# Optimization experiments

Measured on AMD Instinct MI355X. Metric: run time of the kernel, lower is better.

## Reference

```python
import jax, jax.numpy as jnp
import numpy as np

ALPHA = 0.2  # LeakyReLU negative slope
NEG_INF = -9e15  # mask value used by the torch dense GAT layer

def _gat_layer(x, adj, W, a1, a2):
    # x: [N, F], W: [F, Fh], a1/a2: [Fh]
    Wh = x @ W                                   # [N, Fh]
    f1 = Wh @ a1                                 # [N] source scores
    f2 = Wh @ a2                                 # [N] dest scores
    e = jax.nn.leaky_relu(f1[:, None] + f2[None, :], ALPHA)  # [N, N]
    att = jnp.where(adj > 0, e, NEG_INF)
    att = jax.nn.softmax(att, axis=1)
    return att @ Wh                              # [N, Fh]

def setup_inputs():
    key = jax.random.key(0)
    ks = jax.random.split(key, 8)
    N, F, H, Fh, C = 6144, 512, 4, 64, 40
    x = jax.random.normal(ks[0], (N, F), jnp.float32)
    # sparse-ish binary adjacency with self loops (dense storage as in the module)
    adj = (jax.random.uniform(ks[1], (N, N)) < 0.005).astype(jnp.float32)
    adj = jnp.maximum(adj, jnp.eye(N, dtype=jnp.float32))
    s = 1.0 / np.sqrt(Fh)
    W = jax.random.normal(ks[2], (H, F, Fh), jnp.float32) * s
    a1 = jax.random.normal(ks[3], (H, Fh), jnp.float32) * s
    a2 = jax.random.normal(ks[4], (H, Fh), jnp.float32) * s
    so = 1.0 / np.sqrt(C)
    Wo = jax.random.normal(ks[5], (H * Fh, C), jnp.float32) * so
    ao1 = jax.random.normal(ks[6], (C,), jnp.float32) * so
    ao2 = jax.random.normal(ks[7], (C,), jnp.float32) * so
    return {"x": x, "adj": adj, "W": W, "a1": a1, "a2": a2,
            "Wo": Wo, "ao1": ao1, "ao2": ao2}

def reference(x, adj, W, a1, a2, Wo, ao1, ao2):
    N = x.shape[0]
    # multi-head layer (concat=True -> ELU applied inside each head)
    heads = jax.vmap(_gat_layer, in_axes=(None, None, 0, 0, 0))(x, adj, W, a1, a2)  # [H, N, Fh]
    h = jax.nn.elu(heads)
    h = jnp.transpose(h, (1, 0, 2)).reshape(N, -1)   # concat heads -> [N, H*Fh]
    # output attention layer (concat=False), then outer ELU from GAT.forward
    out = jax.nn.elu(_gat_layer(h, adj, Wo, ao1, ao2))  # [N, C]
    return jax.nn.log_softmax(out, axis=1)
```

## Files before the change

### kernel.cpp

```cpp
#include <hip/hip_runtime.h>
#include <stdint.h>

#define N_NODES 6144
#define F_IN 512
#define NHEAD 4
#define FH 64
#define HF 256
#define NCLS 40
#define CAP 192
#define LRELU_ALPHA 0.2f

typedef __bf16 bf16x8 __attribute__((ext_vector_type(8)));
typedef float floatx4 __attribute__((ext_vector_type(4)));
typedef uint16_t u16x8 __attribute__((ext_vector_type(8)));

__device__ __forceinline__ float b2f(uint16_t u){
    union { float f; uint32_t i; } x; x.i = ((uint32_t)u) << 16; return x.f;
}
__device__ __forceinline__ uint16_t f2b(float f){
    union { float f; uint32_t i; } x; x.f = f;
    uint32_t r = x.i + 0x7FFFu + ((x.i >> 16) & 1u);
    return (uint16_t)(r >> 16);
}
__device__ __forceinline__ void cvt_split8(const float* __restrict__ s, bf16x8& hv, bf16x8& lv){
    union { u16x8 u; bf16x8 b; } H, L;
    #pragma unroll
    for (int j = 0; j < 8; j++){
        uint16_t hb = f2b(s[j]);
        H.u[j] = hb;
        L.u[j] = f2b(s[j] - b2f(hb));
    }
    hv = H.b; lv = L.b;
}

__global__ void k_A(const float* __restrict__ adj, const float* __restrict__ x,
                    const float* __restrict__ W, const float* __restrict__ Wo,
                    const float* __restrict__ a1, const float* __restrict__ a2,
                    int* __restrict__ cnt, int* __restrict__ idxbuf,
                    uint16_t* __restrict__ Woth, uint16_t* __restrict__ Wotl,
                    uint16_t* __restrict__ Wh1b, float* __restrict__ f1,
                    float* __restrict__ f2, float* __restrict__ f1o,
                    float* __restrict__ f2o){
    int b = blockIdx.x, t = threadIdx.x;
    if (b < 384){
        __shared__ float sred[2][2][64];
        int w = t >> 6, l = t & 63;
        int bx = b >> 2, h = b & 3;
        int m = l & 15, q = l >> 4;
        int rt0 = bx * 4 + (w & 1) * 2;
        int ctl = (w >> 1) * 2;
        const float* pa0 = x + (size_t)(rt0 * 16 + m) * F_IN + q * 8;
        const float* pa1 = pa0 + 16 * F_IN;
        const float* pb = W + h * 32768 + q * 8 * 64 + ctl * 16 + m;
        floatx4 acc[2][2] = {};
        for (int kc = 0; kc < 16; kc++){
            float av0[8], av1[8], bv0[8], bv1[8];
            *reinterpret_cast<float4*>(av0)     = *reinterpret_cast<const float4*>(pa0 + kc * 32);
            *reinterpret_cast<float4*>(av0 + 4) = *reinterpret_cast<const float4*>(pa0 + kc * 32 + 4);
            *reinterpret_cast<float4*>(av1)     = *reinterpret_cast<const float4*>(pa1 + kc * 32);
            *reinterpret_cast<float4*>(av1 + 4) = *reinterpret_cast<const float4*>(pa1 + kc * 32 + 4);
            const float* pbk = pb + kc * 2048;
            #pragma unroll
            for (int j = 0; j < 8; j++){
                bv0[j] = pbk[j * 64];
                bv1[j] = pbk[j * 64 + 16];
            }
            bf16x8 a0h, a0l, a1h_, a1l_, b0h, b0l, b1h, b1l;
            cvt_split8(av0, a0h, a0l);
            cvt_split8(av1, a1h_, a1l_);
            cvt_split8(bv0, b0h, b0l);
            cvt_split8(bv1, b1h, b1l);
            acc[0][0] = __builtin_amdgcn_mfma_f32_16x16x32_bf16(a0h, b0l, acc[0][0], 0, 0, 0);
            acc[0][0] = __builtin_amdgcn_mfma_f32_16x16x32_bf16(a0l, b0h, acc[0][0], 0, 0, 0);
            acc[0][0] = __builtin_amdgcn_mfma_f32_16x16x32_bf16(a0h, b0h, acc[0][0], 0, 0, 0);
            acc[0][1] = __builtin_amdgcn_mfma_f32_16x16x32_bf16(a0h, b1l, acc[0][1], 0, 0, 0);
            acc[0][1] = __builtin_amdgcn_mfma_f32_16x16x32_bf16(a0l, b1h, acc[0][1], 0, 0, 0);
            acc[0][1] = __builtin_amdgcn_mfma_f32_16x16x32_bf16(a0h, b1h, acc[0][1], 0, 0, 0);
            acc[1][0] = __builtin_amdgcn_mfma_f32_16x16x32_bf16(a1h_, b0l, acc[1][0], 0, 0, 0);
            acc[1][0] = __builtin_amdgcn_mfma_f32_16x16x32_bf16(a1l_, b0h, acc[1][0], 0, 0, 0);
            acc[1][0] = __builtin_amdgcn_mfma_f32_16x16x32_bf16(a1h_, b0h, acc[1][0], 0, 0, 0);
            acc[1][1] = __builtin_amdgcn_mfma_f32_16x16x32_bf16(a1h_, b1l, acc[1][1], 0, 0, 0);
            acc[1][1] = __builtin_amdgcn_mfma_f32_16x16x32_bf16(a1l_, b1h, acc[1][1], 0, 0, 0);
            acc[1][1] = __builtin_amdgcn_mfma_f32_16x16x32_bf16(a1h_, b1h, acc[1][1], 0, 0, 0);
        }
        #pragma unroll
        for (int fr = 0; fr < 2; fr++){
            #pragma unroll
            for (int fc = 0; fc < 2; fc++){
                int col = h * 64 + (ctl + fc) * 16 + m;
                int rowb = (rt0 + fr) * 16 + q * 4;
                #pragma unroll
                for (int r = 0; r < 4; r++)
                    Wh1b[(size_t)(rowb + r) * HF + col] = f2b(acc[fr][fc][r]);
            }
        }
        float a1v0 = a1[h * FH + (ctl + 0) * 16 + m];
        float a1v1 = a1[h * FH + (ctl + 1) * 16 + m];
        float a2v0 = a2[h * FH + (ctl + 0) * 16 + m];
        float a2v1 = a2[h * FH + (ctl + 1) * 16 + m];
        #pragma unroll
        for (int fr = 0; fr < 2; fr++){
            #pragma unroll
            for (int r = 0; r < 4; r++){
                float s1 = acc[fr][0][r] * a1v0 + acc[fr][1][r] * a1v1;
                float s2 = acc[fr][0][r] * a2v0 + acc[fr][1][r] * a2v1;
                #pragma unroll
                for (int off = 1; off < 16; off <<= 1){
                    s1 += __shfl_xor(s1, off);
                    s2 += __shfl_xor(s2, off);
                }
                if (m == 0){
                    int lr = ((w & 1) * 2 + fr) * 16 + q * 4 + r;
                    sred[w >> 1][0][lr] = s1;
                    sred[w >> 1][1][lr] = s2;
                }
            }
        }
        __syncthreads();
        if (t < 64){
            int n = bx * 64 + t;
            f1[h * N_NODES + n] = sred[0][0][t] + sred[1][0][t];
            f2[h * N_NODES + n] = sred[0][1][t] + sred[1][1][t];
        }
    } else if (b < 432){
        int T = (b - 384) * 256 + t;
        int c = T >> 8, k = T & 255;
        float v = (c < NCLS) ? Wo[k * NCLS + c] : 0.f;
        uint16_t hi = f2b(v);
        Woth[c * HF + k] = hi;
        Wotl[c * HF + k] = f2b(v - b2f(hi));
    } else if (b == 432){
        for (int i = t; i < N_NODES; i += 256){ f1o[i] = 0.f; f2o[i] = 0.f; }
    } else {
        __shared__ int scnt;
        int i = b - 433;
        if (t == 0) scnt = 0;
        __syncthreads();
        const float4* row = reinterpret_cast<const float4*>(adj + (size_t)i * N_NODES);
        int* out = idxbuf + (size_t)i * CAP;
        for (int q = t; q < N_NODES / 4; q += 256){
            float4 v = row[q];
            int j0 = q * 4;
            if (v.x != 0.f){ int p = atomicAdd(&scnt, 1); if (p < CAP) out[p] = j0;     }
            if (v.y != 0.f){ int p = atomicAdd(&scnt, 1); if (p < CAP) out[p] = j0 + 1; }
            if (v.z != 0.f){ int p = atomicAdd(&scnt, 1); if (p < CAP) out[p] = j0 + 2; }
            if (v.w != 0.f){ int p = atomicAdd(&scnt, 1); if (p < CAP) out[p] = j0 + 3; }
        }
        __syncthreads();
        if (t == 0) cnt[i] = scnt < CAP ? scnt : CAP;
    }
}

__global__ void k_attn1(const int* __restrict__ cnt, const int* __restrict__ idxbuf,
                        const uint16_t* __restrict__ Wh1b, const float* __restrict__ f1,
                        const float* __restrict__ f2,
                        uint16_t* __restrict__ hch, uint16_t* __restrict__ hcl){
    int i = blockIdx.x, h = threadIdx.x >> 6, l = threadIdx.x & 63;
    int c = cnt[i];
    __shared__ int   sidx[CAP];
    __shared__ float sp[NHEAD][CAP];
    const int* src = idxbuf + (size_t)i * CAP;
    for (int e = threadIdx.x; e < c; e += 256) sidx[e] = src[e];
    __syncthreads();
    float f1i = f1[h * N_NODES + i];
    const float* f2h = f2 + h * N_NODES;
    float mx = -1e30f;
    for (int e = l; e < c; e += 64){
        float s = f1i + f2h[sidx[e]];
        s = s > 0.f ? s : LRELU_ALPHA * s;
        sp[h][e] = s;
        mx = fmaxf(mx, s);
    }
    for (int off = 32; off; off >>= 1) mx = fmaxf(mx, __shfl_xor(mx, off));
    float ssum = 0.f;
    for (int e = l; e < c; e += 64){
        float p = __expf(sp[h][e] - mx);
        sp[h][e] = p;
        ssum += p;
    }
    for (int off = 32; off; off >>= 1) ssum += __shfl_xor(ssum, off);
    float inv = 1.f / ssum;
    float acc = 0.f;
    const uint16_t* whb = Wh1b + h * FH + l;
    int e = 0;
    for (; e + 4 <= c; e += 4){
        int j0 = sidx[e], j1 = sidx[e+1], j2 = sidx[e+2], j3 = sidx[e+3];
        float v0 = b2f(whb[(size_t)j0 * HF]);
        float v1 = b2f(whb[(size_t)j1 * HF]);
        float v2 = b2f(whb[(size_t)j2 * HF]);
        float v3 = b2f(whb[(size_t)j3 * HF]);
        acc += sp[h][e]*v0 + sp[h][e+1]*v1 + sp[h][e+2]*v2 + sp[h][e+3]*v3;
    }
    for (; e < c; e++)
        acc += sp[h][e] * b2f(whb[(size_t)sidx[e] * HF]);
    acc *= inv;
    float v = acc > 0.f ? acc : __expf(acc) - 1.f;
    uint16_t hi = f2b(v);
    uint16_t lo = f2b(v - b2f(hi));
    size_t o = (size_t)i * HF + h * FH + l;
    hch[o] = hi;
    hcl[o] = lo;
}

__global__ void k_gemm2(const uint16_t* __restrict__ hch, const uint16_t* __restrict__ hcl,
                        const uint16_t* __restrict__ Woth, const uint16_t* __restrict__ Wotl,
                        const float* __restrict__ ao1, const float* __restrict__ ao2,
                        float* __restrict__ Wh2, float* __restrict__ f1o,
                        float* __restrict__ f2o){
    int w = threadIdx.x >> 6, l = threadIdx.x & 63;
    int r0 = blockIdx.x * 32 + w * 16;
    int c0 = blockIdx.y * 16;
    int m = l & 15, q = l >> 4;
    const uint16_t* pah = hch  + (size_t)(r0 + m) * HF + q * 8;
    const uint16_t* pal = hcl  + (size_t)(r0 + m) * HF + q * 8;
    const uint16_t* pbh = Woth + (size_t)(c0 + m) * HF + q * 8;
    const uint16_t* pbl = Wotl + (size_t)(c0 + m) * HF + q * 8;
    floatx4 acc = {};
    for (int k0 = 0; k0 < HF; k0 += 32){
        bf16x8 ah = *reinterpret_cast<const bf16x8*>(pah + k0);
        bf16x8 al = *reinterpret_cast<const bf16x8*>(pal + k0);
        bf16x8 bh = *reinterpret_cast<const bf16x8*>(pbh + k0);
        bf16x8 bl = *reinterpret_cast<const bf16x8*>(pbl + k0);
        acc = __builtin_amdgcn_mfma_f32_16x16x32_bf16(ah, bl, acc, 0, 0, 0);
        acc = __builtin_amdgcn_mfma_f32_16x16x32_bf16(al, bh, acc, 0, 0, 0);
        acc = __builtin_amdgcn_mfma_f32_16x16x32_bf16(ah, bh, acc, 0, 0, 0);
    }
    int col = c0 + m;
    bool valid = col < NCLS;
    if (valid){
        int rowb = r0 + q * 4;
        #pragma unroll
        for (int r = 0; r < 4; r++)
            Wh2[(size_t)(rowb + r) * NCLS + col] = acc[r];
    }
    float w1 = valid ? ao1[col] : 0.f;
    float w2 = valid ? ao2[col] : 0.f;
    #pragma unroll
    for (int r = 0; r < 4; r++){
        float s1 = acc[r] * w1;
        float s2 = acc[r] * w2;
        #pragma unroll
        for (int off = 1; off < 16; off <<= 1){
            s1 += __shfl_xor(s1, off);
            s2 += __shfl_xor(s2, off);
        }
        if (m == 0){
            atomicAdd(f1o + r0 + q * 4 + r, s1);
            atomicAdd(f2o + r0 + q * 4 + r, s2);
        }
    }
}

__global__ void k_attn2(const int* __restrict__ cnt, const int* __restrict__ idxbuf,
                        const float* __restrict__ Wh2, const float* __restrict__ f1o,
                        const float* __restrict__ f2o, float* __restrict__ out){
    int i = blockIdx.x, l = threadIdx.x;
    int c = cnt[i];
    __shared__ int   sidx[CAP];
    __shared__ float sp[CAP];
    const int* src = idxbuf + (size_t)i * CAP;
    for (int e = l; e < c; e += 64) sidx[e] = src[e];
    __syncthreads();
    float f1i = f1o[i];
    float mx = -1e30f;
    for (int e = l; e < c; e += 64){
        float s = f1i + f2o[sidx[e]];
        s = s > 0.f ? s : LRELU_ALPHA * s;
        sp[e] = s;
        mx = fmaxf(mx, s);
    }
    for (int off = 32; off; off >>= 1) mx = fmaxf(mx, __shfl_xor(mx, off));
    __syncthreads();
    float ssum = 0.f;
    for (int e = l; e < c; e += 64){
        float p = __expf(sp[e] - mx);
        sp[e] = p;
        ssum += p;
    }
    for (int off = 32; off; off >>= 1) ssum += __shfl_xor(ssum, off);
    float inv = 1.f / ssum;
    __syncthreads();
    float acc = 0.f;
    if (l < NCLS){
        const float* wb = Wh2 + l;
        int e = 0;
        for (; e + 4 <= c; e += 4){
            int j0 = sidx[e], j1 = sidx[e+1], j2 = sidx[e+2], j3 = sidx[e+3];
            float v0 = wb[(size_t)j0 * NCLS];
            float v1 = wb[(size_t)j1 * NCLS];
            float v2 = wb[(size_t)j2 * NCLS];
            float v3 = wb[(size_t)j3 * NCLS];
            acc += sp[e]*v0 + sp[e+1]*v1 + sp[e+2]*v2 + sp[e+3]*v3;
        }
        for (; e < c; e++)
            acc += sp[e] * wb[(size_t)sidx[e] * NCLS];
        acc *= inv;
    }
    float o = (l < NCLS) ? (acc > 0.f ? acc : __expf(acc) - 1.f) : -1e30f;
    float m2 = o;
    for (int off = 32; off; off >>= 1) m2 = fmaxf(m2, __shfl_xor(m2, off));
    float ex = (l < NCLS) ? __expf(o - m2) : 0.f;
    for (int off = 32; off; off >>= 1) ex += __shfl_xor(ex, off);
    float res = o - m2 - logf(ex);
    if (l < NCLS) out[(size_t)i * NCLS + l] = res;
}

extern "C" void kernel_launch(void* const* d_in, const int* in_sizes, int n_in,
                              void* d_out, int out_size, void* d_ws, size_t ws_size,
                              hipStream_t stream) {
    const float* x   = (const float*)d_in[0];
    const float* adj = (const float*)d_in[1];
    const float* W   = (const float*)d_in[2];
    const float* a1  = (const float*)d_in[3];
    const float* a2  = (const float*)d_in[4];
    const float* Wo  = (const float*)d_in[5];
    const float* ao1 = (const float*)d_in[6];
    const float* ao2 = (const float*)d_in[7];
    float* out = (float*)d_out;

    char* ws = (char*)d_ws;
    int*      nbr_cnt = (int*)     (ws + 0);
    int*      nbr_idx = (int*)     (ws + 24576);
    uint16_t* Woth    = (uint16_t*)(ws + 4743168);
    uint16_t* Wotl    = (uint16_t*)(ws + 4767744);
    uint16_t* Wh1b    = (uint16_t*)(ws + 4792320);
    float*    f1      = (float*)   (ws + 7938048);
    float*    f2      = (float*)   (ws + 8036352);
    uint16_t* hch     = (uint16_t*)(ws + 8134656);
    uint16_t* hcl     = (uint16_t*)(ws + 11280384);
    float*    Wh2     = (float*)   (ws + 14426112);
    float*    f1o     = (float*)   (ws + 15409152);
    float*    f2o     = (float*)   (ws + 15433728);

    hipLaunchKernelGGL(k_A,     dim3(6577),   dim3(256), 0, stream, adj, x, W, Wo, a1, a2,
                       nbr_cnt, nbr_idx, Woth, Wotl, Wh1b, f1, f2, f1o, f2o);
    hipLaunchKernelGGL(k_attn1, dim3(6144),   dim3(256), 0, stream, nbr_cnt, nbr_idx,
                       Wh1b, f1, f2, hch, hcl);
    hipLaunchKernelGGL(k_gemm2, dim3(192, 3), dim3(128), 0, stream, hch, hcl, Woth, Wotl,
                       ao1, ao2, Wh2, f1o, f2o);
    hipLaunchKernelGGL(k_attn2, dim3(6144),   dim3(64),  0, stream, nbr_cnt, nbr_idx,
                       Wh2, f1o, f2o, out);
}
```

Before: 271.0 us.

## Fuse four kernels into one persistent kernel with grid-wide barriers

Replaces the four separate launches with a single persistent kernel of 512 blocks that loops over the work items of each former stage and uses atomic-counter grid barriers between stages. This targets launch overhead and the inter-kernel drain/fill gaps. The adjacency scan now does six non-temporal vector loads per thread up front, and the second attention stage packs four nodes per block. The spin barrier assumes all 512 blocks are co-resident, which could deadlock if occupancy is lower. The fixed grid may also underuse the GPU during the memory-bound adjacency scan.

```diff
diff --git a/kernel.cpp b/kernel.cpp
--- a/kernel.cpp
+++ b/kernel.cpp
@@ -9,6 +9,8 @@
 #define NCLS 40
 #define CAP 192
 #define LRELU_ALPHA 0.2f
+#define NB 512
+#define NITEMS_A 6577
 
 typedef __bf16 bf16x8 __attribute__((ext_vector_type(8)));
 typedef float floatx4 __attribute__((ext_vector_type(4)));
@@ -33,276 +35,298 @@
     hv = H.b; lv = L.b;
 }
 
-__global__ void k_A(const float* __restrict__ adj, const float* __restrict__ x,
-                    const float* __restrict__ W, const float* __restrict__ Wo,
-                    const float* __restrict__ a1, const float* __restrict__ a2,
-                    int* __restrict__ cnt, int* __restrict__ idxbuf,
-                    uint16_t* __restrict__ Woth, uint16_t* __restrict__ Wotl,
-                    uint16_t* __restrict__ Wh1b, float* __restrict__ f1,
-                    float* __restrict__ f2, float* __restrict__ f1o,
-                    float* __restrict__ f2o){
-    int b = blockIdx.x, t = threadIdx.x;
-    if (b < 384){
-        __shared__ float sred[2][2][64];
-        int w = t >> 6, l = t & 63;
-        int bx = b >> 2, h = b & 3;
-        int m = l & 15, q = l >> 4;
-        int rt0 = bx * 4 + (w & 1) * 2;
-        int ctl = (w >> 1) * 2;
-        const float* pa0 = x + (size_t)(rt0 * 16 + m) * F_IN + q * 8;
-        const float* pa1 = pa0 + 16 * F_IN;
-        const float* pb = W + h * 32768 + q * 8 * 64 + ctl * 16 + m;
-        floatx4 acc[2][2] = {};
-        for (int kc = 0; kc < 16; kc++){
-            float av0[8], av1[8], bv0[8], bv1[8];
-            *reinterpret_cast<float4*>(av0)     = *reinterpret_cast<const float4*>(pa0 + kc * 32);
-            *reinterpret_cast<float4*>(av0 + 4) = *reinterpret_cast<const float4*>(pa0 + kc * 32 + 4);
-            *reinterpret_cast<float4*>(av1)     = *reinterpret_cast<const float4*>(pa1 + kc * 32);
-            *reinterpret_cast<float4*>(av1 + 4) = *reinterpret_cast<const float4*>(pa1 + kc * 32 + 4);
-            const float* pbk = pb + kc * 2048;
-            #pragma unroll
-            for (int j = 0; j < 8; j++){
-                bv0[j] = pbk[j * 64];
-                bv1[j] = pbk[j * 64 + 16];
-            }
-            bf16x8 a0h, a0l, a1h_, a1l_, b0h, b0l, b1h, b1l;
-            cvt_split8(av0, a0h, a0l);
-            cvt_split8(av1, a1h_, a1l_);
-            cvt_split8(bv0, b0h, b0l);
-            cvt_split8(bv1, b1h, b1l);
-            acc[0][0] = __builtin_amdgcn_mfma_f32_16x16x32_bf16(a0h, b0l, acc[0][0], 0, 0, 0);
-            acc[0][0] = __builtin_amdgcn_mfma_f32_16x16x32_bf16(a0l, b0h, acc[0][0], 0, 0, 0);
-            acc[0][0] = __builtin_amdgcn_mfma_f32_16x16x32_bf16(a0h, b0h, acc[0][0], 0, 0, 0);
-            acc[0][1] = __builtin_amdgcn_mfma_f32_16x16x32_bf16(a0h, b1l, acc[0][1], 0, 0, 0);
-            acc[0][1] = __builtin_amdgcn_mfma_f32_16x16x32_bf16(a0l, b1h, acc[0][1], 0, 0, 0);
-            acc[0][1] = __builtin_amdgcn_mfma_f32_16x16x32_bf16(a0h, b1h, acc[0][1], 0, 0, 0);
-            acc[1][0] = __builtin_amdgcn_mfma_f32_16x16x32_bf16(a1h_, b0l, acc[1][0], 0, 0, 0);
-            acc[1][0] = __builtin_amdgcn_mfma_f32_16x16x32_bf16(a1l_, b0h, acc[1][0], 0, 0, 0);
-            acc[1][0] = __builtin_amdgcn_mfma_f32_16x16x32_bf16(a1h_, b0h, acc[1][0], 0, 0, 0);
-            acc[1][1] = __builtin_amdgcn_mfma_f32_16x16x32_bf16(a1h_, b1l, acc[1][1], 0, 0, 0);
-            acc[1][1] = __builtin_amdgcn_mfma_f32_16x16x32_bf16(a1l_, b1h, acc[1][1], 0, 0, 0);
-            acc[1][1] = __builtin_amdgcn_mfma_f32_16x16x32_bf16(a1h_, b1h, acc[1][1], 0, 0, 0);
-        }
-        #pragma unroll
-        for (int fr = 0; fr < 2; fr++){
-            #pragma unroll
-            for (int fc = 0; fc < 2; fc++){
-                int col = h * 64 + (ctl + fc) * 16 + m;
-                int rowb = (rt0 + fr) * 16 + q * 4;
+__device__ __forceinline__ void gsync(int* bar, int target){
+    __syncthreads();
+    if (threadIdx.x == 0){
+        __threadfence();
+        __hip_atomic_fetch_add(bar, 1, __ATOMIC_RELEASE, __HIP_MEMORY_SCOPE_AGENT);
+        while (__hip_atomic_load(bar, __ATOMIC_ACQUIRE, __HIP_MEMORY_SCOPE_AGENT) < target)
+            __builtin_amdgcn_s_sleep(1);
+        __threadfence();
+    }
+    __syncthreads();
+}
+
+__global__ __launch_bounds__(256, 2) void k_fused(
+    const float* __restrict__ adj, const float* __restrict__ x,
+    const float* __restrict__ W,   const float* __restrict__ Wo,
+    const float* __restrict__ a1,  const float* __restrict__ a2,
+    const float* __restrict__ ao1, const float* __restrict__ ao2,
+    int* __restrict__ cnt, int* __restrict__ idxbuf,
+    uint16_t* __restrict__ Woth, uint16_t* __restrict__ Wotl,
+    uint16_t* __restrict__ Wh1b, float* __restrict__ f1, float* __restrict__ f2,
+    uint16_t* __restrict__ hch, uint16_t* __restrict__ hcl,
+    float* __restrict__ Wh2, float* __restrict__ f1o, float* __restrict__ f2o,
+    float* __restrict__ out, int* __restrict__ bar)
+{
+    const int t = threadIdx.x;
+    __shared__ float sred[2][2][64];
+    __shared__ int   scnt;
+    __shared__ int   sidxB[CAP];
+    __shared__ float spB[NHEAD][CAP];
+    __shared__ int   sidxD[4][CAP];
+    __shared__ float spD[4][CAP];
+
+    for (int b = blockIdx.x; b < NITEMS_A; b += NB){
+        if (b < 384){
+            int w = t >> 6, l = t & 63;
+            int bx = b >> 2, h = b & 3;
+            int m = l & 15, q = l >> 4;
+            int rt0 = bx * 4 + (w & 1) * 2;
+            int ctl = (w >> 1) * 2;
+            const float* pa0 = x + (size_t)(rt0 * 16 + m) * F_IN + q * 8;
+            const float* pa1 = pa0 + 16 * F_IN;
+            const float* pb = W + h * 32768 + q * 8 * 64 + ctl * 16 + m;
+            floatx4 acc[2][2] = {};
+            for (int kc = 0; kc < 16; kc++){
+                float av0[8], av1[8], bv0[8], bv1[8];
+                *reinterpret_cast<float4*>(av0)     = *reinterpret_cast<const float4*>(pa0 + kc * 32);
+                *reinterpret_cast<float4*>(av0 + 4) = *reinterpret_cast<const float4*>(pa0 + kc * 32 + 4);
+                *reinterpret_cast<float4*>(av1)     = *reinterpret_cast<const float4*>(pa1 + kc * 32);
+                *reinterpret_cast<float4*>(av1 + 4) = *reinterpret_cast<const float4*>(pa1 + kc * 32 + 4);
+                const float* pbk = pb + kc * 2048;
                 #pragma unroll
-                for (int r = 0; r < 4; r++)
-                    Wh1b[(size_t)(rowb + r) * HF + col] = f2b(acc[fr][fc][r]);
-            }
-        }
-        float a1v0 = a1[h * FH + (ctl + 0) * 16 + m];
-        float a1v1 = a1[h * FH + (ctl + 1) * 16 + m];
-        float a2v0 = a2[h * FH + (ctl + 0) * 16 + m];
-        float a2v1 = a2[h * FH + (ctl + 1) * 16 + m];
-        #pragma unroll
-        for (int fr = 0; fr < 2; fr++){
-            #pragma unroll
-            for (int r = 0; r < 4; r++){
-                float s1 = acc[fr][0][r] * a1v0 + acc[fr][1][r] * a1v1;
-                float s2 = acc[fr][0][r] * a2v0 + acc[fr][1][r] * a2v1;
+                for (int j = 0; j < 8; j++){
+                    bv0[j] = pbk[j * 64];
+                    bv1[j] = pbk[j * 64 + 16];
+                }
+                bf16x8 a0h, a0l, a1h_, a1l_, b0h, b0l, b1h, b1l;
+                cvt_split8(av0, a0h, a0l);
+                cvt_split8(av1, a1h_, a1l_);
+                cvt_split8(bv0, b0h, b0l);
+                cvt_split8(bv1, b1h, b1l);
+                acc[0][0] = __builtin_amdgcn_mfma_f32_16x16x32_bf16(a0h, b0l, acc[0][0], 0, 0, 0);
+                acc[0][0] = __builtin_amdgcn_mfma_f32_16x16x32_bf16(a0l, b0h, acc[0][0], 0, 0, 0);
+                acc[0][0] = __builtin_amdgcn_mfma_f32_16x16x32_bf16(a0h, b0h, acc[0][0], 0, 0, 0);
+                acc[0][1] = __builtin_amdgcn_mfma_f32_16x16x32_bf16(a0h, b1l, acc[0][1], 0, 0, 0);
+                acc[0][1] = __builtin_amdgcn_mfma_f32_16x16x32_bf16(a0l, b1h, acc[0][1], 0, 0, 0);
+                acc[0][1] = __builtin_amdgcn_mfma_f32_16x16x32_bf16(a0h, b1h, acc[0][1], 0, 0, 0);
+                acc[1][0] = __builtin_amdgcn_mfma_f32_16x16x32_bf16(a1h_, b0l, acc[1][0], 0, 0, 0);
+                acc[1][0] = __builtin_amdgcn_mfma_f32_16x16x32_bf16(a1l_, b0h, acc[1][0], 0, 0, 0);
+                acc[1][0] = __builtin_amdgcn_mfma_f32_16x16x32_bf16(a1h_, b0h, acc[1][0], 0, 0, 0);
+                acc[1][1] = __builtin_amdgcn_mfma_f32_16x16x32_bf16(a1h_, b1l, acc[1][1], 0, 0, 0);
+                acc[1][1] = __builtin_amdgcn_mfma_f32_16x16x32_bf16(a1l_, b1h, acc[1][1], 0, 0, 0);
+                acc[1][1] = __builtin_amdgcn_mfma_f32_16x16x32_bf16(a1h_, b1h, acc[1][1], 0, 0, 0);
+            }
+            #pragma unroll
+            for (int fr = 0; fr < 2; fr++){
                 #pragma unroll
-                for (int off = 1; off < 16; off <<= 1){
-                    s1 += __shfl_xor(s1, off);
-                    s2 += __shfl_xor(s2, off);
+                for (int fc = 0; fc < 2; fc++){
+                    int col = h * 64 + (ctl + fc) * 16 + m;
+                    int rowb = (rt0 + fr) * 16 + q * 4;
+                    #pragma unroll
+                    for (int r = 0; r < 4; r++)
+                        Wh1b[(size_t)(rowb + r) * HF + col] = f2b(acc[fr][fc][r]);
                 }
-                if (m == 0){
-                    int lr = ((w & 1) * 2 + fr) * 16 + q * 4 + r;
-                    sred[w >> 1][0][lr] = s1;
-                    sred[w >> 1][1][lr] = s2;
+            }
+            float a1v0 = a1[h * FH + (ctl + 0) * 16 + m];
+            float a1v1 = a1[h * FH + (ctl + 1) * 16 + m];
+            float a2v0 = a2[h * FH + (ctl + 0) * 16 + m];
+            float a2v1 = a2[h * FH + (ctl + 1) * 16 + m];
+            #pragma unroll
+            for (int fr = 0; fr < 2; fr++){
+                #pragma unroll
+                for (int r = 0; r < 4; r++){
+                    float s1 = acc[fr][0][r] * a1v0 + acc[fr][1][r] * a1v1;
+                    float s2 = acc[fr][0][r] * a2v0 + acc[fr][1][r] * a2v1;
+                    #pragma unroll
+                    for (int off = 1; off < 16; off <<= 1){
+                        s1 += __shfl_xor(s1, off);
+                        s2 += __shfl_xor(s2, off);
+                    }
+                    if (m == 0){
+                        int lr = ((w & 1) * 2 + fr) * 16 + q * 4 + r;
+                        sred[w >> 1][0][lr] = s1;
+                        sred[w >> 1][1][lr] = s2;
+                    }
                 }
             }
+            __syncthreads();
+            if (t < 64){
+                int n = bx * 64 + t;
+                f1[h * N_NODES + n] = sred[0][0][t] + sred[1][0][t];
+                f2[h * N_NODES + n] = sred[0][1][t] + sred[1][1][t];
+            }
+        } else if (b < 432){
+            int T = (b - 384) * 256 + t;
+            int c = T >> 8, k = T & 255;
+            float v = (c < NCLS) ? Wo[k * NCLS + c] : 0.f;
+            uint16_t hi = f2b(v);
+            Woth[c * HF + k] = hi;
+            Wotl[c * HF + k] = f2b(v - b2f(hi));
+        } else if (b == 432){
+            for (int i = t; i < N_NODES; i += 256){ f1o[i] = 0.f; f2o[i] = 0.f; }
+        } else {
+            int i = b - 433;
+            if (t == 0) scnt = 0;
+            __syncthreads();
+            const floatx4* row = reinterpret_cast<const floatx4*>(adj + (size_t)i * N_NODES);
+            int* outp = idxbuf + (size_t)i * CAP;
+            floatx4 v[6];
+            #pragma unroll
+            for (int u = 0; u < 6; u++)
+                v[u] = __builtin_nontemporal_load(row + t + u * 256);
+            #pragma unroll
+            for (int u = 0; u < 6; u++){
+                int j0 = (t + u * 256) * 4;
+                if (v[u][0] != 0.f){ int p = atomicAdd(&scnt, 1); if (p < CAP) outp[p] = j0;     }
+                if (v[u][1] != 0.f){ int p = atomicAdd(&scnt, 1); if (p < CAP) outp[p] = j0 + 1; }
+                if (v[u][2] != 0.f){ int p = atomicAdd(&scnt, 1); if (p < CAP) outp[p] = j0 + 2; }
+                if (v[u][3] != 0.f){ int p = atomicAdd(&scnt, 1); if (p < CAP) outp[p] = j0 + 3; }
+            }
+            __syncthreads();
+            if (t == 0) cnt[i] = scnt < CAP ? scnt : CAP;
         }
         __syncthreads();
-        if (t < 64){
-            int n = bx * 64 + t;
-            f1[h * N_NODES + n] = sred[0][0][t] + sred[1][0][t];
-            f2[h * N_NODES + n] = sred[0][1][t] + sred[1][1][t];
-        }
-    } else if (b < 432){
-        int T = (b - 384) * 256 + t;
-        int c = T >> 8, k = T & 255;
-        float v = (c < NCLS) ? Wo[k * NCLS + c] : 0.f;
-        uint16_t hi = f2b(v);
-        Woth[c * HF + k] = hi;
-        Wotl[c * HF + k] = f2b(v - b2f(hi));
-    } else if (b == 432){
-        for (int i = t; i < N_NODES; i += 256){ f1o[i] = 0.f; f2o[i] = 0.f; }
-    } else {
-        __shared__ int scnt;
-        int i = b - 433;
-        if (t == 0) scnt = 0;
+    }
+    gsync(bar, NB);
+
+    for (int i = blockIdx.x; i < N_NODES; i += NB){
+        int h = t >> 6, l = t & 63;
+        int c = cnt[i];
+        const int* src = idxbuf + (size_t)i * CAP;
+        for (int e = t; e < c; e += 256) sidxB[e] = src[e];
         __syncthreads();
-        const float4* row = reinterpret_cast<const float4*>(adj + (size_t)i * N_NODES);
-        int* out = idxbuf + (size_t)i * CAP;
-        for (int q = t; q < N_NODES / 4; q += 256){
-            float4 v = row[q];
-            int j0 = q * 4;
-            if (v.x != 0.f){ int p = atomicAdd(&scnt, 1); if (p < CAP) out[p] = j0;     }
-            if (v.y != 0.f){ int p = atomicAdd(&scnt, 1); if (p < CAP) out[p] = j0 + 1; }
-            if (v.z != 0.f){ int p = atomicAdd(&scnt, 1); if (p < CAP) out[p] = j0 + 2; }
-            if (v.w != 0.f){ int p = atomicAdd(&scnt, 1); if (p < CAP) out[p] = j0 + 3; }
-        }
-        __syncthreads();
-        if (t == 0) cnt[i] = scnt < CAP ? scnt : CAP;
-    }
-}
-
-__global__ void k_attn1(const int* __restrict__ cnt, const int* __restrict__ idxbuf,
-                        const uint16_t* __restrict__ Wh1b, const float* __restrict__ f1,
-                        const float* __restrict__ f2,
-                        uint16_t* __restrict__ hch, uint16_t* __restrict__ hcl){
-    int i = blockIdx.x, h = threadIdx.x >> 6, l = threadIdx.x & 63;
-    int c = cnt[i];
-    __shared__ int   sidx[CAP];
-    __shared__ float sp[NHEAD][CAP];
-    const int* src = idxbuf + (size_t)i * CAP;
-    for (int e = threadIdx.x; e < c; e += 256) sidx[e] = src[e];
-    __syncthreads();
-    float f1i = f1[h * N_NODES + i];
-    const float* f2h = f2 + h * N_NODES;
-    float mx = -1e30f;
-    for (int e = l; e < c; e += 64){
-        float s = f1i + f2h[sidx[e]];
-        s = s > 0.f ? s : LRELU_ALPHA * s;
-        sp[h][e] = s;
-        mx = fmaxf(mx, s);
-    }
-    for (int off = 32; off; off >>= 1) mx = fmaxf(mx, __shfl_xor(mx, off));
-    float ssum = 0.f;
-    for (int e = l; e < c; e += 64){
-        float p = __expf(sp[h][e] - mx);
-        sp[h][e] = p;
-        ssum += p;
-    }
-    for (int off = 32; off; off >>= 1) ssum += __shfl_xor(ssum, off);
-    float inv = 1.f / ssum;
-    float acc = 0.f;
-    const uint16_t* whb = Wh1b + h * FH + l;
-    int e = 0;
-    for (; e + 4 <= c; e += 4){
-        int j0 = sidx[e], j1 = sidx[e+1], j2 = sidx[e+2], j3 = sidx[e+3];
-        float v0 = b2f(whb[(size_t)j0 * HF]);
-        float v1 = b2f(whb[(size_t)j1 * HF]);
-        float v2 = b2f(whb[(size_t)j2 * HF]);
-        float v3 = b2f(whb[(size_t)j3 * HF]);
-        acc += sp[h][e]*v0 + sp[h][e+1]*v1 + sp[h][e+2]*v2 + sp[h][e+3]*v3;
-    }
-    for (; e < c; e++)
-        acc += sp[h][e] * b2f(whb[(size_t)sidx[e] * HF]);
-    acc *= inv;
-    float v = acc > 0.f ? acc : __expf(acc) - 1.f;
-    uint16_t hi = f2b(v);
-    uint16_t lo = f2b(v - b2f(hi));
-    size_t o = (size_t)i * HF + h * FH + l;
-    hch[o] = hi;
-    hcl[o] = lo;
-}
-
-__global__ void k_gemm2(const uint16_t* __restrict__ hch, const uint16_t* __restrict__ hcl,
-                        const uint16_t* __restrict__ Woth, const uint16_t* __restrict__ Wotl,
-                        const float* __restrict__ ao1, const float* __restrict__ ao2,
-                        float* __restrict__ Wh2, float* __restrict__ f1o,
-                        float* __restrict__ f2o){
-    int w = threadIdx.x >> 6, l = threadIdx.x & 63;
-    int r0 = blockIdx.x * 32 + w * 16;
-    int c0 = blockIdx.y * 16;
-    int m = l & 15, q = l >> 4;
-    const uint16_t* pah = hch  + (size_t)(r0 + m) * HF + q * 8;
-    const uint16_t* pal = hcl  + (size_t)(r0 + m) * HF + q * 8;
-    const uint16_t* pbh = Woth + (size_t)(c0 + m) * HF + q * 8;
-    const uint16_t* pbl = Wotl + (size_t)(c0 + m) * HF + q * 8;
-    floatx4 acc = {};
-    for (int k0 = 0; k0 < HF; k0 += 32){
-        bf16x8 ah = *reinterpret_cast<const bf16x8*>(pah + k0);
-        bf16x8 al = *reinterpret_cast<const bf16x8*>(pal + k0);
-        bf16x8 bh = *reinterpret_cast<const bf16x8*>(pbh + k0);
-        bf16x8 bl = *reinterpret_cast<const bf16x8*>(pbl + k0);
-        acc = __builtin_amdgcn_mfma_f32_16x16x32_bf16(ah, bl, acc, 0, 0, 0);
-        acc = __builtin_amdgcn_mfma_f32_16x16x32_bf16(al, bh, acc, 0, 0, 0);
-        acc = __builtin_amdgcn_mfma_f32_16x16x32_bf16(ah, bh, acc, 0, 0, 0);
-    }
-    int col = c0 + m;
-    bool valid = col < NCLS;
-    if (valid){
-        int rowb = r0 + q * 4;
-        #pragma unroll
-        for (int r = 0; r < 4; r++)
-            Wh2[(size_t)(rowb + r) * NCLS + col] = acc[r];
-    }
-    float w1 = valid ? ao1[col] : 0.f;
-    float w2 = valid ? ao2[col] : 0.f;
-    #pragma unroll
-    for (int r = 0; r < 4; r++){
-        float s1 = acc[r] * w1;
-        float s2 = acc[r] * w2;
-        #pragma unroll
-        for (int off = 1; off < 16; off <<= 1){
-            s1 += __shfl_xor(s1, off);
-            s2 += __shfl_xor(s2, off);
-        }
-        if (m == 0){
-            atomicAdd(f1o + r0 + q * 4 + r, s1);
-            atomicAdd(f2o + r0 + q * 4 + r, s2);
-        }
-    }
-}
-
-__global__ void k_attn2(const int* __restrict__ cnt, const int* __restrict__ idxbuf,
-                        const float* __restrict__ Wh2, const float* __restrict__ f1o,
-                        const float* __restrict__ f2o, float* __restrict__ out){
-    int i = blockIdx.x, l = threadIdx.x;
-    int c = cnt[i];
-    __shared__ int   sidx[CAP];
-    __shared__ float sp[CAP];
-    const int* src = idxbuf + (size_t)i * CAP;
-    for (int e = l; e < c; e += 64) sidx[e] = src[e];
-    __syncthreads();
-    float f1i = f1o[i];
-    float mx = -1e30f;
-    for (int e = l; e < c; e += 64){
-        float s = f1i + f2o[sidx[e]];
-        s = s > 0.f ? s : LRELU_ALPHA * s;
-        sp[e] = s;
-        mx = fmaxf(mx, s);
-    }
-    for (int off = 32; off; off >>= 1) mx = fmaxf(mx, __shfl_xor(mx, off));
-    __syncthreads();
-    float ssum = 0.f;
-    for (int e = l; e < c; e += 64){
-        float p = __expf(sp[e] - mx);
-        sp[e] = p;
-        ssum += p;
-    }
-    for (int off = 32; off; off >>= 1) ssum += __shfl_xor(ssum, off);
-    float inv = 1.f / ssum;
-    __syncthreads();
-    float acc = 0.f;
-    if (l < NCLS){
-        const float* wb = Wh2 + l;
+        float f1i = f1[h * N_NODES + i];
+        const float* f2h = f2 + h * N_NODES;
+        float mx = -1e30f;
+        for (int e = l; e < c; e += 64){
+            float s = f1i + f2h[sidxB[e]];
+            s = s > 0.f ? s : LRELU_ALPHA * s;
+            spB[h][e] = s;
+            mx = fmaxf(mx, s);
+        }
+        for (int off = 32; off; off >>= 1) mx = fmaxf(mx, __shfl_xor(mx, off));
+        float ssum = 0.f;
+        for (int e = l; e < c; e += 64){
+            float p = __expf(spB[h][e] - mx);
+            spB[h][e] = p;
+            ssum += p;
+        }
+        for (int off = 32; off; off >>= 1) ssum += __shfl_xor(ssum, off);
+        float inv = 1.f / ssum;
+        float acc = 0.f;
+        const uint16_t* whb = Wh1b + h * FH + l;
         int e = 0;
         for (; e + 4 <= c; e += 4){
-            int j0 = sidx[e], j1 = sidx[e+1], j2 = sidx[e+2], j3 = sidx[e+3];
-            float v0 = wb[(size_t)j0 * NCLS];
-            float v1 = wb[(size_t)j1 * NCLS];
-            float v2 = wb[(size_t)j2 * NCLS];
-            float v3 = wb[(size_t)j3 * NCLS];
-            acc += sp[e]*v0 + sp[e+1]*v1 + sp[e+2]*v2 + sp[e+3]*v3;
+            int j0 = sidxB[e], j1 = sidxB[e+1], j2 = sidxB[e+2], j3 = sidxB[e+3];
+            float v0 = b2f(whb[(size_t)j0 * HF]);
+            float v1 = b2f(whb[(size_t)j1 * HF]);
+            float v2 = b2f(whb[(size_t)j2 * HF]);
+            float v3 = b2f(whb[(size_t)j3 * HF]);
+            acc += spB[h][e]*v0 + spB[h][e+1]*v1 + spB[h][e+2]*v2 + spB[h][e+3]*v3;
         }
         for (; e < c; e++)
-            acc += sp[e] * wb[(size_t)sidx[e] * NCLS];
+            acc += spB[h][e] * b2f(whb[(size_t)sidxB[e] * HF]);
         acc *= inv;
-    }
-    float o = (l < NCLS) ? (acc > 0.f ? acc : __expf(acc) - 1.f) : -1e30f;
-    float m2 = o;
-    for (int off = 32; off; off >>= 1) m2 = fmaxf(m2, __shfl_xor(m2, off));
-    float ex = (l < NCLS) ? __expf(o - m2) : 0.f;
-    for (int off = 32; off; off >>= 1) ex += __shfl_xor(ex, off);
-    float res = o - m2 - logf(ex);
-    if (l < NCLS) out[(size_t)i * NCLS + l] = res;
+        float v = acc > 0.f ? acc : __expf(acc) - 1.f;
+        uint16_t hi = f2b(v);
+        uint16_t lo = f2b(v - b2f(hi));
+        size_t o = (size_t)i * HF + h * FH + l;
+        hch[o] = hi;
+        hcl[o] = lo;
+        __syncthreads();
+    }
+    gsync(bar, 2 * NB);
+
+    for (int ib = blockIdx.x; ib < 288; ib += NB){
+        int T  = ib * 2 + (t >> 7);
+        int lt = t & 127;
+        int w = lt >> 6, l = lt & 63;
+        int bx = T / 3, by = T % 3;
+        int r0 = bx * 32 + w * 16;
+        int c0 = by * 16;
+        int m = l & 15, q = l >> 4;
+        const uint16_t* pah = hch  + (size_t)(r0 + m) * HF + q * 8;
+        const uint16_t* pal = hcl  + (size_t)(r0 + m) * HF + q * 8;
+        const uint16_t* pbh = Woth + (size_t)(c0 + m) * HF + q * 8;
+        const uint16_t* pbl = Wotl + (size_t)(c0 + m) * HF + q * 8;
+        floatx4 acc = {};
+        for (int k0 = 0; k0 < HF; k0 += 32){
+            bf16x8 ah = *reinterpret_cast<const bf16x8*>(pah + k0);
+            bf16x8 al = *reinterpret_cast<const bf16x8*>(pal + k0);
+            bf16x8 bh = *reinterpret_cast<const bf16x8*>(pbh + k0);
+            bf16x8 bl = *reinterpret_cast<const bf16x8*>(pbl + k0);
+            acc = __builtin_amdgcn_mfma_f32_16x16x32_bf16(ah, bl, acc, 0, 0, 0);
+            acc = __builtin_amdgcn_mfma_f32_16x16x32_bf16(al, bh, acc, 0, 0, 0);
+            acc = __builtin_amdgcn_mfma_f32_16x16x32_bf16(ah, bh, acc, 0, 0, 0);
+        }
+        int col = c0 + m;
+        bool valid = col < NCLS;
+        if (valid){
+            int rowb = r0 + q * 4;
+            #pragma unroll
+            for (int r = 0; r < 4; r++)
+                Wh2[(size_t)(rowb + r) * NCLS + col] = acc[r];
+        }
+        float w1 = valid ? ao1[col] : 0.f;
+        float w2 = valid ? ao2[col] : 0.f;
+        #pragma unroll
+        for (int r = 0; r < 4; r++){
+            float s1 = acc[r] * w1;
+            float s2 = acc[r] * w2;
+            #pragma unroll
+            for (int off = 1; off < 16; off <<= 1){
+                s1 += __shfl_xor(s1, off);
+                s2 += __shfl_xor(s2, off);
+            }
+            if (m == 0){
+                atomicAdd(f1o + r0 + q * 4 + r, s1);
+                atomicAdd(f2o + r0 + q * 4 + r, s2);
+            }
+        }
+    }
+    gsync(bar, 3 * NB);
+
+    for (int ib = blockIdx.x; ib < 1536; ib += NB){
+        int w = t >> 6, l = t & 63;
+        int i = ib * 4 + w;
+        int c = cnt[i];
+        int*   sidx = sidxD[w];
+        float* sp   = spD[w];
+        const int* src = idxbuf + (size_t)i * CAP;
+        for (int e = l; e < c; e += 64) sidx[e] = src[e];
+        float f1i = f1o[i];
+        float mx = -1e30f;
+        for (int e = l; e < c; e += 64){
+            float s = f1i + f2o[sidx[e]];
+            s = s > 0.f ? s : LRELU_ALPHA * s;
+            sp[e] = s;
+            mx = fmaxf(mx, s);
+        }
+        for (int off = 32; off; off >>= 1) mx = fmaxf(mx, __shfl_xor(mx, off));
+        float ssum = 0.f;
+        for (int e = l; e < c; e += 64){
+            float p = __expf(sp[e] - mx);
+            sp[e] = p;
+            ssum += p;
+        }
+        for (int off = 32; off; off >>= 1) ssum += __shfl_xor(ssum, off);
+        float inv = 1.f / ssum;
+        float acc = 0.f;
+        if (l < NCLS){
+            const float* wb = Wh2 + l;
+            int e = 0;
+            for (; e + 4 <= c; e += 4){
+                int j0 = sidx[e], j1 = sidx[e+1], j2 = sidx[e+2], j3 = sidx[e+3];
+                float v0 = wb[(size_t)j0 * NCLS];
+                float v1 = wb[(size_t)j1 * NCLS];
+                float v2 = wb[(size_t)j2 * NCLS];
+                float v3 = wb[(size_t)j3 * NCLS];
+                acc += sp[e]*v0 + sp[e+1]*v1 + sp[e+2]*v2 + sp[e+3]*v3;
+            }
+            for (; e < c; e++)
+                acc += sp[e] * wb[(size_t)sidx[e] * NCLS];
+            acc *= inv;
+        }
+        float o = (l < NCLS) ? (acc > 0.f ? acc : __expf(acc) - 1.f) : -1e30f;
+        float m2 = o;
+        for (int off = 32; off; off >>= 1) m2 = fmaxf(m2, __shfl_xor(m2, off));
+        float ex = (l < NCLS) ? __expf(o - m2) : 0.f;
+        for (int off = 32; off; off >>= 1) ex += __shfl_xor(ex, off);
+        float res = o - m2 - logf(ex);
+        if (l < NCLS) out[(size_t)i * NCLS + l] = res;
+    }
 }
 
 extern "C" void kernel_launch(void* const* d_in, const int* in_sizes, int n_in,
@@ -331,13 +355,11 @@
     float*    Wh2     = (float*)   (ws + 14426112);
     float*    f1o     = (float*)   (ws + 15409152);
     float*    f2o     = (float*)   (ws + 15433728);
-
-    hipLaunchKernelGGL(k_A,     dim3(6577),   dim3(256), 0, stream, adj, x, W, Wo, a1, a2,
-                       nbr_cnt, nbr_idx, Woth, Wotl, Wh1b, f1, f2, f1o, f2o);
-    hipLaunchKernelGGL(k_attn1, dim3(6144),   dim3(256), 0, stream, nbr_cnt, nbr_idx,
-                       Wh1b, f1, f2, hch, hcl);
-    hipLaunchKernelGGL(k_gemm2, dim3(192, 3), dim3(128), 0, stream, hch, hcl, Woth, Wotl,
-                       ao1, ao2, Wh2, f1o, f2o);
-    hipLaunchKernelGGL(k_attn2, dim3(6144),   dim3(64),  0, stream, nbr_cnt, nbr_idx,
-                       Wh2, f1o, f2o, out);
-}
+    int*      bar     = (int*)     (ws + 15458304);
+
+    hipMemsetAsync(bar, 0, 64, stream);
+    hipLaunchKernelGGL(k_fused, dim3(NB), dim3(256), 0, stream,
+                       adj, x, W, Wo, a1, a2, ao1, ao2,
+                       nbr_cnt, nbr_idx, Woth, Wotl, Wh1b, f1, f2,
+                       hch, hcl, Wh2, f1o, f2o, out, bar);
+}
```

New measurement: 602.3 us. +122.2%, slower.
